# Kernel tuning notes

Hardware: AMD Instinct MI355X
Metric: run time of the kernel (lower is better)

The kernel has to match this reference:

```python
import jax, jax.numpy as jnp
import numpy as np
from math import sqrt

MUL = 256        # multiplicity of every irrep slot
N = 20000        # batch (edges/nodes)
FS = MUL * 1 * MUL  # flat size of each uvw weight path (u=256, v=1, w=256)

def _cg_tensors():
    # real-basis Wigner-3j (Clebsch-Gordan) tensors for l <= 1, e3nn normalization (sum of squares = 1)
    C000 = np.ones((1, 1, 1))
    eye3 = np.eye(3) / sqrt(3.0)
    C011 = eye3.reshape(1, 3, 3)
    C101 = eye3.reshape(3, 1, 3)
    C110 = eye3.reshape(3, 3, 1)
    eps = np.zeros((3, 3, 3))
    eps[0, 1, 2] = eps[1, 2, 0] = eps[2, 0, 1] = 1.0
    eps[0, 2, 1] = eps[2, 1, 0] = eps[1, 0, 2] = -1.0
    C111 = eps / sqrt(6.0)
    return C000, C011, C101, C110, C111

_C000, _C011, _C101, _C110, _C111 = [jnp.asarray(c, dtype=jnp.float32) for c in _cg_tensors()]

# normalization: alpha = sqrt((2*l_out+1) / sum_{paths with same i_out} mul1*mul2)
_A0 = sqrt(1.0 / (2 * MUL))   # l_out=0: dim 1, fan sum = 256+256 = 512
_A1 = sqrt(3.0 / (3 * MUL))   # l_out=1: dim 3, fan sum = 256*3 = 768

# (i_in1, i_in2, i_out, CG, alpha) — order defines weight layout
PATHS = [
    (0, 0, 0, _C000, _A0),
    (0, 1, 1, _C011, _A1),
    (1, 0, 1, _C101, _A1),
    (1, 1, 0, _C110, _A0),
    (1, 1, 1, _C111, _A1),
]

def setup_inputs() -> dict:
    key = jax.random.key(0)
    k1, k2, k3 = jax.random.split(key, 3)
    x1 = jax.random.normal(k1, (N, 4 * MUL), dtype=jnp.float32)   # 256x0e (256) + 256x1e (768)
    x2 = jax.random.normal(k2, (N, 4), dtype=jnp.float32)         # 1x0e (1) + 1x1e (3)
    w = jax.random.normal(k3, (5 * FS,), dtype=jnp.float32)
    # rescale=True: scale init weights by 1/sqrt(slices_fan_in[i_out]); fan_in(uvw)=mul1*mul2=256
    k0 = 1.0 / sqrt(2 * MUL)   # i_out=0: 256+256
    k1_ = 1.0 / sqrt(3 * MUL)  # i_out=1: 256*3
    scales = jnp.concatenate([jnp.full((FS,), s, dtype=jnp.float32) for s in (k0, k1_, k1_, k0, k1_)])
    weight = w * scales
    return {"x1": x1, "x2": x2, "weight": weight}

def reference(x1, x2, weight):
    n = x1.shape[0]
    x1_segs = (x1[:, :MUL].reshape(n, MUL, 1), x1[:, MUL:].reshape(n, MUL, 3))
    x2_segs = (x2[:, :1].reshape(n, 1, 1), x2[:, 1:].reshape(n, 1, 3))
    outs = [jnp.zeros((n, MUL, 1), x1.dtype), jnp.zeros((n, MUL, 3), x1.dtype)]
    off = 0
    for (ia, ib, io, cg, alpha) in PATHS:
        w = weight[off:off + FS].reshape(MUL, 1, MUL)
        off += FS
        outs[io] = outs[io] + alpha * jnp.einsum('uvw,ijk,zui,zvj->zwk', w, cg, x1_segs[ia], x2_segs[ib])
    return jnp.concatenate([outs[0].reshape(n, MUL), outs[1].reshape(n, 3 * MUL)], axis=-1)
```

## Files before the change

kernel.cpp:

```cpp
#include <hip/hip_runtime.h>


typedef short bf16x8 __attribute__((ext_vector_type(8)));
typedef float f32x4 __attribute__((ext_vector_type(4)));
typedef int   ni4   __attribute__((ext_vector_type(4)));

static __device__ __forceinline__ unsigned short f2bf(float f) {
  unsigned int u = __builtin_bit_cast(unsigned int, f);
  u += 0x7FFFu + ((u >> 16) & 1u);
  return (unsigned short)(u >> 16);
}

static __device__ __forceinline__ bf16x8 asbf(int4 v) {
  return __builtin_bit_cast(bf16x8, v);
}
static __device__ __forceinline__ bf16x8 asbfn(ni4 v) {
  return __builtin_bit_cast(bf16x8, v);
}

static __device__ __forceinline__ void gload4(ni4& dst, const void* p) {
  asm volatile("global_load_dwordx4 %0, %1, off" : "=v"(dst) : "v"(p));
}

#define WAITV(n) do { \
    asm volatile("s_waitcnt vmcnt(" #n ")"); \
    __builtin_amdgcn_sched_barrier(0); \
  } while (0)

static __device__ __forceinline__ void phase_barrier() {
  __builtin_amdgcn_sched_barrier(0);
  asm volatile("s_waitcnt lgkmcnt(0)");
  __builtin_amdgcn_sched_barrier(0);
  __builtin_amdgcn_s_barrier();
  __builtin_amdgcn_sched_barrier(0);
}

__global__ __launch_bounds__(256) void prep_weights(
    const float* __restrict__ wgt, unsigned short* __restrict__ Bw)
{
  int fid = blockIdx.x * 256 + threadIdx.x;
  union { unsigned short h[8]; int4 v; } pk;
  if (fid < 24576) {
    int lane = fid & 63;
    int ct = (fid >> 6) & 15;
    int q = fid >> 10;
    int kt = q % 6, c = q / 6;
    int w = ct * 16 + (lane & 15);
    int kh = (lane >> 4) * 8;
#pragma unroll
    for (int e = 0; e < 8; ++e) {
      int kc = kt * 32 + kh + e;
      int seg = kc >> 6;
      int u = c * 64 + (kc & 63);
      float s  = (seg == 2) ? 0.025515518153991442f : 0.03608439182435161f;
      int off  = (seg == 0) ? 65536 : (seg == 1 ? 131072 : 262144);
      pk.h[e] = f2bf(wgt[off + u * 256 + w] * s);
    }
    ((int4*)Bw)[fid] = pk.v;
  } else if (fid < 40960) {
    int f2 = fid - 24576;
    int lane = f2 & 63;
    int ct = (f2 >> 6) & 15;
    int q = f2 >> 10;
    int kt = q & 3, c = q >> 2;
    int w = ct * 16 + (lane & 15);
    int kh = (lane >> 4) * 8;
#pragma unroll
    for (int e = 0; e < 8; ++e) {
      int kc = kt * 32 + kh + e;
      int seg = kc >> 6;
      int u = c * 64 + (kc & 63);
      float s  = (seg == 0) ? 0.04419417382415922f : 0.025515518153991442f;
      int off  = (seg == 0) ? 0 : 196608;
      pk.h[e] = f2bf(wgt[off + u * 256 + w] * s);
    }
    ((int4*)Bw)[fid] = pk.v;
  }
}

#define BUFSLOTS 1408
#define T0BASE 1152

struct X1Raw { ni4 a0, a1, a2, a3; };

static __device__ __forceinline__ void load_x1_asm(
    X1Raw& r, const float* __restrict__ x1, int zrow, int ub, int rr)
{
  const float* base = x1 + (size_t)zrow * 1024;
  gload4(r.a0, base + ub + rr * 4);
  const float* pv = base + 256 + 3 * ub + rr * 12;
  gload4(r.a1, pv);
  gload4(r.a2, pv + 4);
  gload4(r.a3, pv + 8);
}

static __device__ __forceinline__ void build_frags(
    const X1Raw& r, int zl, int rr, float s2, const float* v2, int4* ldsT)
{
  union { float4 q; float f[4]; } s1u;
  s1u.q = __builtin_bit_cast(float4, r.a0);
  union { float4 q[3]; float f[12]; } v1u;
  v1u.q[0] = __builtin_bit_cast(float4, r.a1);
  v1u.q[1] = __builtin_bit_cast(float4, r.a2);
  v1u.q[2] = __builtin_bit_cast(float4, r.a3);
  const int lh   = (rr >> 1) & 3;
  const int kq   = rr >> 3;
  const int half = rr & 1;
  int2* lds2 = (int2*)ldsT;

#pragma unroll
  for (int sg = 0; sg < 3; ++sg) {
#pragma unroll
    for (int k = 0; k < 3; ++k) {
      int row = 3 * zl + k;
      int kt  = sg * 2 + kq;
      int fl  = (((lh << 4) | (row & 15)) ^ (kt & 7)) ^ lh;
      int slot = (row >> 4) * 384 + kt * 64 + fl;
      float t[4];
      if (sg == 0) {
#pragma unroll
        for (int e = 0; e < 4; ++e) t[e] = s1u.f[e] * v2[k];
      } else if (sg == 1) {
#pragma unroll
        for (int e = 0; e < 4; ++e) t[e] = v1u.f[3 * e + k] * s2;
      } else {
        int k1 = k + 1; if (k1 > 2) k1 -= 3;
        int k2 = k + 2; if (k2 > 2) k2 -= 3;
#pragma unroll
        for (int e = 0; e < 4; ++e)
          t[e] = v1u.f[3 * e + k1] * v2[k2] - v1u.f[3 * e + k2] * v2[k1];
      }
      union { unsigned short h[4]; int2 v; } pk;
#pragma unroll
      for (int e = 0; e < 4; ++e) pk.h[e] = f2bf(t[e]);
      lds2[slot * 2 + half] = pk.v;
    }
  }
#pragma unroll
  for (int sg = 0; sg < 2; ++sg) {
    int kt = sg * 2 + kq;
    int fl = (((lh << 4) | zl) ^ (kt & 7)) ^ lh;
    int slot = T0BASE + kt * 64 + fl;
    float t[4];
    if (sg == 0) {
#pragma unroll
      for (int e = 0; e < 4; ++e) t[e] = s1u.f[e] * s2;
    } else {
#pragma unroll
      for (int e = 0; e < 4; ++e)
        t[e] = v1u.f[3 * e] * v2[0] + v1u.f[3 * e + 1] * v2[1]
             + v1u.f[3 * e + 2] * v2[2];
    }
    union { unsigned short h[4]; int2 v; } pk;
#pragma unroll
    for (int e = 0; e < 4; ++e) pk.h[e] = f2bf(t[e]);
    lds2[slot * 2 + half] = pk.v;
  }
}

static __device__ __forceinline__ void burstB(
    ni4 (&vb)[20], const int4* __restrict__ B1v,
    const int4* __restrict__ B0v, int c, int ct0, int lane)
{
#pragma unroll
  for (int s = 0; s < 6; ++s) {
    const int4* p = B1v + ((size_t)((c * 6 + s) * 16 + ct0)) * 64 + lane;
    gload4(vb[s * 2],     p);
    gload4(vb[s * 2 + 1], p + 64);
  }
#pragma unroll
  for (int s = 0; s < 4; ++s) {
    const int4* p = B0v + ((size_t)((c * 4 + s) * 16 + ct0)) * 64 + lane;
    gload4(vb[12 + s * 2],     p);
    gload4(vb[12 + s * 2 + 1], p + 64);
  }
}

static __device__ __forceinline__ void gemm_steps(
    const int4* __restrict__ buf, const ni4 (&vb)[20], int lane,
    f32x4 acc1[3][2], f32x4 acc0[2])
{
#pragma unroll
  for (int kt = 0; kt < 6; ++kt) {
    int fl = (lane ^ (kt & 7)) ^ (lane >> 4);
    int4 a0 = buf[kt * 64 + fl];
    int4 a1 = buf[384 + kt * 64 + fl];
    int4 a2 = buf[768 + kt * 64 + fl];
    int4 a[3] = {a0, a1, a2};
#pragma unroll
    for (int rt = 0; rt < 3; ++rt) {
      bf16x8 av = asbf(a[rt]);
#pragma unroll
      for (int j = 0; j < 2; ++j)
        acc1[rt][j] = __builtin_amdgcn_mfma_f32_16x16x32_bf16(
            av, asbfn(vb[kt * 2 + j]), acc1[rt][j], 0, 0, 0);
    }
  }
#pragma unroll
  for (int kt = 0; kt < 4; ++kt) {
    int fl = (lane ^ (kt & 7)) ^ (lane >> 4);
    int4 a0 = buf[T0BASE + kt * 64 + fl];
    bf16x8 av = asbf(a0);
#pragma unroll
    for (int j = 0; j < 2; ++j)
      acc0[j] = __builtin_amdgcn_mfma_f32_16x16x32_bf16(
          av, asbfn(vb[12 + kt * 2 + j]), acc0[j], 0, 0, 0);
  }
}

__global__ __launch_bounds__(256, 2) void tp_main(
    const float* __restrict__ x1, const float* __restrict__ x2,
    const int4* __restrict__ B1v, const int4* __restrict__ B0v,
    float* __restrict__ out)
{
  __shared__ int4 ldsT[2 * BUFSLOTS];
  const int tid  = threadIdx.x;
  const int lane = tid & 63;
  const int wid  = tid >> 6;
  const int wh   = blockIdx.x & 1;
  const int ct0  = wh * 8 + wid * 2;
  const int z0   = (blockIdx.x >> 1) * 16;
  const int zl   = tid >> 4;
  const int rr   = tid & 15;

  f32x4 acc1[3][2];
  f32x4 acc0[2];
#pragma unroll
  for (int i = 0; i < 3; ++i)
#pragma unroll
    for (int j = 0; j < 2; ++j) acc1[i][j] = (f32x4){0.f, 0.f, 0.f, 0.f};
#pragma unroll
  for (int j = 0; j < 2; ++j) acc0[j] = (f32x4){0.f, 0.f, 0.f, 0.f};

  float4 x2v = ((const float4*)x2)[z0 + zl];
  const float s2 = x2v.x;
  float v2[3] = {x2v.y, x2v.z, x2v.w};

  X1Raw rA, rB;
  ni4 vb[20];

  load_x1_asm(rA, x1, z0 + zl, 0, rr);
  load_x1_asm(rB, x1, z0 + zl, 64, rr);
  WAITV(4);
  build_frags(rA, zl, rr, s2, v2, ldsT);
  phase_barrier();

  burstB(vb, B1v, B0v, 0, ct0, lane);
  load_x1_asm(rA, x1, z0 + zl, 128, rr);
  WAITV(14);
  build_frags(rB, zl, rr, s2, v2, ldsT + BUFSLOTS);
  WAITV(4);
  gemm_steps(ldsT, vb, lane, acc1, acc0);
  phase_barrier();

  burstB(vb, B1v, B0v, 1, ct0, lane);
  load_x1_asm(rB, x1, z0 + zl, 192, rr);
  WAITV(14);
  build_frags(rA, zl, rr, s2, v2, ldsT);
  WAITV(4);
  gemm_steps(ldsT + BUFSLOTS, vb, lane, acc1, acc0);
  phase_barrier();

  burstB(vb, B1v, B0v, 2, ct0, lane);
  WAITV(10);
  build_frags(rB, zl, rr, s2, v2, ldsT + BUFSLOTS);
  WAITV(0);
  gemm_steps(ldsT, vb, lane, acc1, acc0);
  phase_barrier();

  burstB(vb, B1v, B0v, 3, ct0, lane);
  WAITV(0);
  gemm_steps(ldsT + BUFSLOTS, vb, lane, acc1, acc0);

  const int col = lane & 15;
  const int rb  = (lane >> 4) * 4;
#pragma unroll
  for (int j = 0; j < 2; ++j) {
    int w = (ct0 + j) * 16 + col;
#pragma unroll
    for (int rg = 0; rg < 4; ++rg) {
      int row = rb + rg;
      out[(size_t)(z0 + row) * 1024 + w] = acc0[j][rg];
    }
  }
#pragma unroll
  for (int rt = 0; rt < 3; ++rt) {
#pragma unroll
    for (int j = 0; j < 2; ++j) {
      int w = (ct0 + j) * 16 + col;
#pragma unroll
      for (int rg = 0; rg < 4; ++rg) {
        int row = rt * 16 + rb + rg;
        int zz = row / 3;
        int k  = row - zz * 3;
        out[(size_t)(z0 + zz) * 1024 + 256 + w * 3 + k] = acc1[rt][j][rg];
      }
    }
  }
}

extern "C" void kernel_launch(void* const* d_in, const int* in_sizes, int n_in,
                              void* d_out, int out_size, void* d_ws, size_t ws_size,
                              hipStream_t stream) {
  const float* x1  = (const float*)d_in[0];
  const float* x2  = (const float*)d_in[1];
  const float* wgt = (const float*)d_in[2];
  float* out = (float*)d_out;

  unsigned short* Bw = (unsigned short*)d_ws;
  const int4* B1v = (const int4*)Bw;
  const int4* B0v = B1v + 24576;

  int n = in_sizes[0] / 1024;

  prep_weights<<<160, 256, 0, stream>>>(wgt, Bw);
  tp_main<<<(n / 16) * 2, 256, 0, stream>>>(x1, x2, B1v, B0v, out);
}
```

Before: 73.78 us.

## Process 32 rows per block to double weight reuse, single-buffer LDS

Each block now handles 32 batch rows instead of 16. Every B-weight fragment loaded from global memory therefore feeds twice as many MFMAs, which halves total weight traffic and the block count. The double-buffered A tile becomes a single larger buffer with barriers around each build/gemm phase. MFMA sections are also wrapped in s_setprio. The trade-off is more accumulator and x1 staging registers per thread, plus lost overlap between fragment building and the GEMM that the double buffering used to provide.

Measured after the change: 74.99 us. About the same (+1.6%).

```diff
diff --git a/kernel.cpp b/kernel.cpp
--- a/kernel.cpp
+++ b/kernel.cpp
@@ -78,35 +78,33 @@
   }
 }
 
-#define BUFSLOTS 1408
-#define T0BASE 1152
-
-struct X1Raw { ni4 a0, a1, a2, a3; };
+#define T0BASE 2304
+
+struct X1Raw { ni4 a[8]; };
 
 static __device__ __forceinline__ void load_x1_asm(
     X1Raw& r, const float* __restrict__ x1, int zrow, int ub, int rr)
 {
   const float* base = x1 + (size_t)zrow * 1024;
-  gload4(r.a0, base + ub + rr * 4);
-  const float* pv = base + 256 + 3 * ub + rr * 12;
-  gload4(r.a1, pv);
-  gload4(r.a2, pv + 4);
-  gload4(r.a3, pv + 8);
+  const float* ps = base + ub + rr * 8;
+  gload4(r.a[0], ps);
+  gload4(r.a[1], ps + 4);
+  const float* pv = base + 256 + 3 * ub + rr * 24;
+#pragma unroll
+  for (int i = 0; i < 6; ++i) gload4(r.a[2 + i], pv + 4 * i);
 }
 
 static __device__ __forceinline__ void build_frags(
     const X1Raw& r, int zl, int rr, float s2, const float* v2, int4* ldsT)
 {
-  union { float4 q; float f[4]; } s1u;
-  s1u.q = __builtin_bit_cast(float4, r.a0);
-  union { float4 q[3]; float f[12]; } v1u;
-  v1u.q[0] = __builtin_bit_cast(float4, r.a1);
-  v1u.q[1] = __builtin_bit_cast(float4, r.a2);
-  v1u.q[2] = __builtin_bit_cast(float4, r.a3);
-  const int lh   = (rr >> 1) & 3;
-  const int kq   = rr >> 3;
-  const int half = rr & 1;
-  int2* lds2 = (int2*)ldsT;
+  union { float4 q[2]; float f[8]; } s1u;
+  s1u.q[0] = __builtin_bit_cast(float4, r.a[0]);
+  s1u.q[1] = __builtin_bit_cast(float4, r.a[1]);
+  union { float4 q[6]; float f[24]; } v1u;
+#pragma unroll
+  for (int i = 0; i < 6; ++i) v1u.q[i] = __builtin_bit_cast(float4, r.a[2 + i]);
+  const int lh = rr & 3;
+  const int kq = rr >> 2;
 
 #pragma unroll
   for (int sg = 0; sg < 3; ++sg) {
@@ -115,46 +113,47 @@
       int row = 3 * zl + k;
       int kt  = sg * 2 + kq;
       int fl  = (((lh << 4) | (row & 15)) ^ (kt & 7)) ^ lh;
-      int slot = (row >> 4) * 384 + kt * 64 + fl;
-      float t[4];
+      int addr = (row >> 4) * 384 + kt * 64 + fl;
+      float t[8];
       if (sg == 0) {
 #pragma unroll
-        for (int e = 0; e < 4; ++e) t[e] = s1u.f[e] * v2[k];
+        for (int e = 0; e < 8; ++e) t[e] = s1u.f[e] * v2[k];
       } else if (sg == 1) {
 #pragma unroll
-        for (int e = 0; e < 4; ++e) t[e] = v1u.f[3 * e + k] * s2;
+        for (int e = 0; e < 8; ++e) t[e] = v1u.f[3 * e + k] * s2;
       } else {
         int k1 = k + 1; if (k1 > 2) k1 -= 3;
         int k2 = k + 2; if (k2 > 2) k2 -= 3;
 #pragma unroll
-        for (int e = 0; e < 4; ++e)
+        for (int e = 0; e < 8; ++e)
           t[e] = v1u.f[3 * e + k1] * v2[k2] - v1u.f[3 * e + k2] * v2[k1];
       }
-      union { unsigned short h[4]; int2 v; } pk;
-#pragma unroll
-      for (int e = 0; e < 4; ++e) pk.h[e] = f2bf(t[e]);
-      lds2[slot * 2 + half] = pk.v;
+      union { unsigned short h[8]; int4 v; } pk;
+#pragma unroll
+      for (int e = 0; e < 8; ++e) pk.h[e] = f2bf(t[e]);
+      ldsT[addr] = pk.v;
     }
   }
 #pragma unroll
   for (int sg = 0; sg < 2; ++sg) {
     int kt = sg * 2 + kq;
-    int fl = (((lh << 4) | zl) ^ (kt & 7)) ^ lh;
-    int slot = T0BASE + kt * 64 + fl;
-    float t[4];
+    int fl = (((lh << 4) | (zl & 15)) ^ (kt & 7)) ^ lh;
+    int addr = T0BASE + (zl >> 4) * 256 + kt * 64 + fl;
+    float t[8];
     if (sg == 0) {
 #pragma unroll
-      for (int e = 0; e < 4; ++e) t[e] = s1u.f[e] * s2;
+      for (int e = 0; e < 8; ++e) t[e] = s1u.f[e] * s2;
     } else {
 #pragma unroll
-      for (int e = 0; e < 4; ++e)
-        t[e] = v1u.f[3 * e] * v2[0] + v1u.f[3 * e + 1] * v2[1]
-             + v1u.f[3 * e + 2] * v2[2];
-    }
-    union { unsigned short h[4]; int2 v; } pk;
-#pragma unroll
-    for (int e = 0; e < 4; ++e) pk.h[e] = f2bf(t[e]);
-    lds2[slot * 2 + half] = pk.v;
+      for (int e = 0; e < 8; ++e) {
+        const float* p = v1u.f + 3 * e;
+        t[e] = p[0] * v2[0] + p[1] * v2[1] + p[2] * v2[2];
+      }
+    }
+    union { unsigned short h[8]; int4 v; } pk;
+#pragma unroll
+    for (int e = 0; e < 8; ++e) pk.h[e] = f2bf(t[e]);
+    ldsT[addr] = pk.v;
   }
 }
 
@@ -178,17 +177,17 @@
 
 static __device__ __forceinline__ void gemm_steps(
     const int4* __restrict__ buf, const ni4 (&vb)[20], int lane,
-    f32x4 acc1[3][2], f32x4 acc0[2])
-{
+    f32x4 acc1[6][2], f32x4 acc0[2][2])
+{
+  __builtin_amdgcn_s_setprio(1);
 #pragma unroll
   for (int kt = 0; kt < 6; ++kt) {
     int fl = (lane ^ (kt & 7)) ^ (lane >> 4);
-    int4 a0 = buf[kt * 64 + fl];
-    int4 a1 = buf[384 + kt * 64 + fl];
-    int4 a2 = buf[768 + kt * 64 + fl];
-    int4 a[3] = {a0, a1, a2};
-#pragma unroll
-    for (int rt = 0; rt < 3; ++rt) {
+    int4 a[6];
+#pragma unroll
+    for (int rt = 0; rt < 6; ++rt) a[rt] = buf[rt * 384 + kt * 64 + fl];
+#pragma unroll
+    for (int rt = 0; rt < 6; ++rt) {
       bf16x8 av = asbf(a[rt]);
 #pragma unroll
       for (int j = 0; j < 2; ++j)
@@ -200,12 +199,18 @@
   for (int kt = 0; kt < 4; ++kt) {
     int fl = (lane ^ (kt & 7)) ^ (lane >> 4);
     int4 a0 = buf[T0BASE + kt * 64 + fl];
-    bf16x8 av = asbf(a0);
-#pragma unroll
-    for (int j = 0; j < 2; ++j)
-      acc0[j] = __builtin_amdgcn_mfma_f32_16x16x32_bf16(
-          av, asbfn(vb[12 + kt * 2 + j]), acc0[j], 0, 0, 0);
-  }
+    int4 a1 = buf[T0BASE + 256 + kt * 64 + fl];
+    int4 a[2] = {a0, a1};
+#pragma unroll
+    for (int rt = 0; rt < 2; ++rt) {
+      bf16x8 av = asbf(a[rt]);
+#pragma unroll
+      for (int j = 0; j < 2; ++j)
+        acc0[rt][j] = __builtin_amdgcn_mfma_f32_16x16x32_bf16(
+            av, asbfn(vb[12 + kt * 2 + j]), acc0[rt][j], 0, 0, 0);
+    }
+  }
+  __builtin_amdgcn_s_setprio(0);
 }
 
 __global__ __launch_bounds__(256, 2) void tp_main(
@@ -213,78 +218,89 @@
     const int4* __restrict__ B1v, const int4* __restrict__ B0v,
     float* __restrict__ out)
 {
-  __shared__ int4 ldsT[2 * BUFSLOTS];
+  __shared__ int4 ldsT[2816];
   const int tid  = threadIdx.x;
   const int lane = tid & 63;
   const int wid  = tid >> 6;
   const int wh   = blockIdx.x & 1;
   const int ct0  = wh * 8 + wid * 2;
-  const int z0   = (blockIdx.x >> 1) * 16;
-  const int zl   = tid >> 4;
-  const int rr   = tid & 15;
-
-  f32x4 acc1[3][2];
-  f32x4 acc0[2];
-#pragma unroll
-  for (int i = 0; i < 3; ++i)
+  const int z0   = (blockIdx.x >> 1) * 32;
+  const int zl   = tid >> 3;
+  const int rr   = tid & 7;
+
+  f32x4 acc1[6][2];
+  f32x4 acc0[2][2];
+#pragma unroll
+  for (int i = 0; i < 6; ++i)
 #pragma unroll
     for (int j = 0; j < 2; ++j) acc1[i][j] = (f32x4){0.f, 0.f, 0.f, 0.f};
 #pragma unroll
-  for (int j = 0; j < 2; ++j) acc0[j] = (f32x4){0.f, 0.f, 0.f, 0.f};
-
-  float4 x2v = ((const float4*)x2)[z0 + zl];
+  for (int i = 0; i < 2; ++i)
+#pragma unroll
+    for (int j = 0; j < 2; ++j) acc0[i][j] = (f32x4){0.f, 0.f, 0.f, 0.f};
+
+  ni4 x2raw;
+  gload4(x2raw, x2 + (size_t)(z0 + zl) * 4);
+  WAITV(0);
+  float4 x2v = __builtin_bit_cast(float4, x2raw);
   const float s2 = x2v.x;
   float v2[3] = {x2v.y, x2v.z, x2v.w};
 
-  X1Raw rA, rB;
+  X1Raw rX;
   ni4 vb[20];
 
-  load_x1_asm(rA, x1, z0 + zl, 0, rr);
-  load_x1_asm(rB, x1, z0 + zl, 64, rr);
-  WAITV(4);
-  build_frags(rA, zl, rr, s2, v2, ldsT);
-  phase_barrier();
+  load_x1_asm(rX, x1, z0 + zl, 0, rr);
 
   burstB(vb, B1v, B0v, 0, ct0, lane);
-  load_x1_asm(rA, x1, z0 + zl, 128, rr);
-  WAITV(14);
-  build_frags(rB, zl, rr, s2, v2, ldsT + BUFSLOTS);
-  WAITV(4);
+  WAITV(20);
+  build_frags(rX, zl, rr, s2, v2, ldsT);
+  load_x1_asm(rX, x1, z0 + zl, 64, rr);
+  phase_barrier();
+  WAITV(8);
   gemm_steps(ldsT, vb, lane, acc1, acc0);
   phase_barrier();
 
   burstB(vb, B1v, B0v, 1, ct0, lane);
-  load_x1_asm(rB, x1, z0 + zl, 192, rr);
-  WAITV(14);
-  build_frags(rA, zl, rr, s2, v2, ldsT);
-  WAITV(4);
-  gemm_steps(ldsT + BUFSLOTS, vb, lane, acc1, acc0);
+  WAITV(20);
+  build_frags(rX, zl, rr, s2, v2, ldsT);
+  load_x1_asm(rX, x1, z0 + zl, 128, rr);
+  phase_barrier();
+  WAITV(8);
+  gemm_steps(ldsT, vb, lane, acc1, acc0);
   phase_barrier();
 
   burstB(vb, B1v, B0v, 2, ct0, lane);
-  WAITV(10);
-  build_frags(rB, zl, rr, s2, v2, ldsT + BUFSLOTS);
+  WAITV(20);
+  build_frags(rX, zl, rr, s2, v2, ldsT);
+  load_x1_asm(rX, x1, z0 + zl, 192, rr);
+  phase_barrier();
+  WAITV(8);
+  gemm_steps(ldsT, vb, lane, acc1, acc0);
+  phase_barrier();
+
+  burstB(vb, B1v, B0v, 3, ct0, lane);
+  WAITV(20);
+  build_frags(rX, zl, rr, s2, v2, ldsT);
+  phase_barrier();
   WAITV(0);
   gemm_steps(ldsT, vb, lane, acc1, acc0);
-  phase_barrier();
-
-  burstB(vb, B1v, B0v, 3, ct0, lane);
-  WAITV(0);
-  gemm_steps(ldsT + BUFSLOTS, vb, lane, acc1, acc0);
 
   const int col = lane & 15;
   const int rb  = (lane >> 4) * 4;
 #pragma unroll
-  for (int j = 0; j < 2; ++j) {
-    int w = (ct0 + j) * 16 + col;
-#pragma unroll
-    for (int rg = 0; rg < 4; ++rg) {
-      int row = rb + rg;
-      out[(size_t)(z0 + row) * 1024 + w] = acc0[j][rg];
-    }
-  }
-#pragma unroll
-  for (int rt = 0; rt < 3; ++rt) {
+  for (int rt = 0; rt < 2; ++rt) {
+#pragma unroll
+    for (int j = 0; j < 2; ++j) {
+      int w = (ct0 + j) * 16 + col;
+#pragma unroll
+      for (int rg = 0; rg < 4; ++rg) {
+        int row = rt * 16 + rb + rg;
+        out[(size_t)(z0 + row) * 1024 + w] = acc0[rt][j][rg];
+      }
+    }
+  }
+#pragma unroll
+  for (int rt = 0; rt < 6; ++rt) {
 #pragma unroll
     for (int j = 0; j < 2; ++j) {
       int w = (ct0 + j) * 16 + col;
@@ -314,5 +330,5 @@
   int n = in_sizes[0] / 1024;
 
   prep_weights<<<160, 256, 0, stream>>>(wgt, Bw);
-  tp_main<<<(n / 16) * 2, 256, 0, stream>>>(x1, x2, B1v, B0v, out);
-}
+  tp_main<<<(n / 32) * 2, 256, 0, stream>>>(x1, x2, B1v, B0v, out);
+}
```
